# Kernel tuning notes

Measured on AMD Instinct MI355X. Metric: run time of the kernel, lower is better.

Reference implementation:

```python
import jax, jax.numpy as jnp
import numpy as np

D = 1024   # embd_dim
H = 4      # number of SelectiveAttentionModule heads (each full-dim)
B, S = 4, 2048


def _layernorm(x, g, b, eps=1e-5):
    mu = jnp.mean(x, axis=-1, keepdims=True)
    var = jnp.var(x, axis=-1, keepdims=True)
    return (x - mu) * jax.lax.rsqrt(var + eps) * g + b


def setup_inputs() -> dict:
    key = jax.random.key(0)
    ks = jax.random.split(key, 16)
    sd = 1.0 / np.sqrt(D)
    x = jax.random.normal(ks[0], (B, S, D), dtype=jnp.float32)
    # per-head Q/K/V projections, stacked over head dim H ([H, in, out] layout)
    Wq = jax.random.uniform(ks[1], (H, D, D), jnp.float32, -sd, sd)
    bq = jax.random.uniform(ks[2], (H, D), jnp.float32, -sd, sd)
    Wk = jax.random.uniform(ks[3], (H, D, D), jnp.float32, -sd, sd)
    bk = jax.random.uniform(ks[4], (H, D), jnp.float32, -sd, sd)
    Wv = jax.random.uniform(ks[5], (H, D, D), jnp.float32, -sd, sd)
    bv = jax.random.uniform(ks[6], (H, D), jnp.float32, -sd, sd)
    sd1 = 1.0 / np.sqrt(H * D)
    W1 = jax.random.uniform(ks[7], (H * D, D), jnp.float32, -sd1, sd1)  # [in, out]
    b1 = jax.random.uniform(ks[8], (D,), jnp.float32, -sd1, sd1)
    W2 = jax.random.uniform(ks[9], (D, D), jnp.float32, -sd, sd)
    b2 = jax.random.uniform(ks[10], (D,), jnp.float32, -sd, sd)
    g1 = jnp.ones((D,), jnp.float32)
    be1 = jnp.zeros((D,), jnp.float32)
    g2 = jnp.ones((D,), jnp.float32)
    be2 = jnp.zeros((D,), jnp.float32)
    return {"embedding_matrix": x, "Wq": Wq, "bq": bq, "Wk": Wk, "bk": bk,
            "Wv": Wv, "bv": bv, "W1": W1, "b1": b1, "g1": g1, "be1": be1,
            "W2": W2, "b2": b2, "g2": g2, "be2": be2}


def reference(embedding_matrix, Wq, bq, Wk, bk, Wv, bv, W1, b1, g1, be1, W2, b2, g2, be2):
    x = embedding_matrix  # [B, S, D]
    # batched per-head projections: [H, B, S, D]
    q = jnp.einsum('bsd,hde->hbse', x, Wq) + bq[:, None, None, :]
    k = jnp.einsum('bsd,hde->hbse', x, Wk) + bk[:, None, None, :]
    v = jnp.einsum('bsd,hde->hbse', x, Wv) + bv[:, None, None, :]
    scale = 1.0 / jnp.sqrt(jnp.asarray(D, x.dtype))
    scores = jnp.einsum('hbse,hbte->hbst', q, k) * scale  # [H, B, S, S]
    attn = jax.nn.softmax(scores, axis=-1)
    heads = jnp.einsum('hbst,hbte->hbse', attn, v)        # [H, B, S, D]
    # torch.cat([V1..V4], dim=-1) == heads reordered to [B, S, H*D]
    concat = jnp.moveaxis(heads, 0, 2).reshape(x.shape[0], x.shape[1], H * D)
    proj = concat @ W1 + b1                               # [B, S, D]
    y = _layernorm(x + proj, g1, be1)
    return _layernorm(y + (y @ W2 + b2), g2, be2)
```

## Files before the change

### kernel.cpp

```cpp
#include <hip/hip_runtime.h>

using u16 = unsigned short;
using u32 = unsigned int;
typedef __attribute__((ext_vector_type(8))) short s16x8;
typedef __attribute__((ext_vector_type(4))) float f32x4;

typedef uint4   __attribute__((may_alias)) uint4a;
typedef ushort4 __attribute__((may_alias)) ushort4a;
typedef float4  __attribute__((may_alias)) float4a;
typedef u16     __attribute__((may_alias)) u16a;
typedef s16x8   __attribute__((may_alias)) s16x8a;

#define D_ 1024
#define H_ 4
#define B_ 4
#define S_ 2048
#define M_ 8192

#define BM 128
#define BN 128
#define BK 32

__device__ __forceinline__ float bf2f(u16 u) { return __uint_as_float(((u32)u) << 16); }
__device__ __forceinline__ u16 f2bf(float f) {
  u32 b = __float_as_uint(f);
  return (u16)((b + 0x7fffu + ((b >> 16) & 1u)) >> 16);
}

__device__ __forceinline__ void gload_lds16(const u16* g, u16* l) {
  __builtin_amdgcn_global_load_lds(
      (const __attribute__((address_space(1))) void*)g,
      (__attribute__((address_space(3))) void*)l, 16, 0, 0);
}

#define FENCE asm volatile("" ::: "memory")
#define BAR do { FENCE; __builtin_amdgcn_s_barrier(); FENCE; } while (0)
#define VMC8 asm volatile("s_waitcnt vmcnt(8)" ::: "memory")
#define VMC4 asm volatile("s_waitcnt vmcnt(4)" ::: "memory")
#define VMC0 asm volatile("s_waitcnt vmcnt(0)" ::: "memory")
#define LGKM0 do { asm volatile("s_waitcnt lgkmcnt(0)" ::: "memory"); \
                   __builtin_amdgcn_sched_barrier(0); } while (0)

__device__ __forceinline__ void swz_decomp(int& x, int& y, int& z) {
  const int gx = gridDim.x, gy = gridDim.y;
  const int nwg = gx * gy * gridDim.z;
  const int flat = (blockIdx.z * gy + blockIdx.y) * gx + blockIdx.x;
  const int swz = (flat & 7) * (nwg >> 3) + (flat >> 3);
  const int t = swz >> 4, i = swz & 15;
  const int tiles_X = (gx * gridDim.z) >> 2;
  const int X = (t % tiles_X) * 4 + (i & 3);
  y = (t / tiles_X) * 4 + (i >> 2);
  z = X / gx;
  x = X % gx;
}

__global__ __launch_bounds__(256) void cvt_f32_bf16(const float* __restrict__ in,
                                                    u16* __restrict__ out, long n4) {
  long stride = (long)gridDim.x * blockDim.x;
  for (long i = (long)blockIdx.x * blockDim.x + threadIdx.x; i < n4; i += stride) {
    float4 v = ((const float4a*)in)[i];
    ushort4 o;
    o.x = f2bf(v.x); o.y = f2bf(v.y); o.z = f2bf(v.z); o.w = f2bf(v.w);
    ((ushort4a*)out)[i] = o;
  }
}

__global__ __launch_bounds__(256) void tcvt(const float* __restrict__ in,
                                            u16* __restrict__ out, int K, int N,
                                            long s_in, long s_out) {
  __shared__ float t[32][33];
  const int z = blockIdx.z;
  in += (long)z * s_in;
  out += (long)z * s_out;
  const int n0 = blockIdx.x * 32, k0 = blockIdx.y * 32;
  const int tx = threadIdx.x & 31, ty = threadIdx.x >> 5;
#pragma unroll
  for (int i = 0; i < 32; i += 8) t[ty + i][tx] = in[(long)(k0 + ty + i) * N + n0 + tx];
  __syncthreads();
#pragma unroll
  for (int i = 0; i < 32; i += 8)
    out[(long)(n0 + ty + i) * K + k0 + tx] = f2bf(t[tx][ty + i]);
}

__global__ __launch_bounds__(256) void biascat(const float* __restrict__ bq,
                                               const float* __restrict__ bk,
                                               const float* __restrict__ bv,
                                               float* __restrict__ o) {
  int i = blockIdx.x * 256 + threadIdx.x;
  float v = (i < 4096) ? bq[i] : ((i < 8192) ? bk[i - 4096] : bv[i - 8192]);
  o[i] = v;
}

__device__ __forceinline__ s16x8 lds_frag(const u16* buf, int r, int jc) {
  return *(const s16x8a*)&buf[(((r << 3) + (jc ^ (r & 7)))) << 3];
}
__device__ __forceinline__ void readB(const u16* Bbuf, int wc, int lane, s16x8 (&bfr)[4][2]) {
#pragma unroll
  for (int j = 0; j < 4; ++j)
#pragma unroll
    for (int s = 0; s < 2; ++s)
      bfr[j][s] = lds_frag(Bbuf, wc * 64 + j * 16 + (lane & 15), 4 * s + (lane >> 4));
}
__device__ __forceinline__ void readA(const u16* Abuf, int q, int wr, int lane, s16x8 (&afr)[2][2]) {
#pragma unroll
  for (int il = 0; il < 2; ++il)
#pragma unroll
    for (int s = 0; s < 2; ++s)
      afr[il][s] = lds_frag(Abuf, wr * 128 + (q * 2 + il) * 16 + (lane & 15), 4 * s + (lane >> 4));
}
__device__ __forceinline__ void mfma_quad(const s16x8 (&afr)[2][2], const s16x8 (&bfr)[4][2],
                                          f32x4 (&acc)[8][4], int q) {
  __builtin_amdgcn_s_setprio(1);
#pragma unroll
  for (int s = 0; s < 2; ++s)
#pragma unroll
    for (int il = 0; il < 2; ++il)
#pragma unroll
      for (int j = 0; j < 4; ++j)
        acc[q * 2 + il][j] =
            __builtin_amdgcn_mfma_f32_16x16x32_bf16(afr[il][s], bfr[j][s], acc[q * 2 + il][j], 0, 0, 0);
  __builtin_amdgcn_s_setprio(0);
}

template <int MODE>
__device__ __forceinline__ void g256_body(
    const u16* __restrict__ A, const u16* __restrict__ Bm, u16* __restrict__ Cp,
    const float* __restrict__ bias, const float* __restrict__ bias2,
    float* __restrict__ dpart, int ldc, long sA, long sB, long sC) {
  __shared__ u16 Al[2][16384];
  __shared__ u16 Bl[2][16384];
  const int bx = blockIdx.x, by = blockIdx.y, z = blockIdx.z;
  A += (long)z * sA;
  Bm += (long)z * sB;
  const long coff = (long)z * sC;
  const int bm = by * 256, bn = bx * 256;
  const int tid = threadIdx.x;
  const int lane = tid & 63;
  const int w = tid >> 6;
  const int wr = w >> 2, wc = w & 3;
  f32x4 acc[8][4] = {};
  const int nt2 = D_ >> 7;

  auto stage = [&](const u16* src, int b0, u16* lbuf, int h, int kt) {
    const int k0 = kt << 6;
#pragma unroll
    for (int it = 0; it < 2; ++it) {
      int c = w * 128 + it * 64 + lane;
      int row = h * 128 + (c >> 3);
      int j = (c & 7) ^ (row & 7);
      gload_lds16(src + (long)(b0 + row) * D_ + (k0 + j * 8),
                  lbuf + ((h * 1024 + w * 128 + it * 64) << 3));
    }
  };

  stage(A, bm, Al[0], 0, 0);
  stage(A, bm, Al[0], 1, 0);
  stage(Bm, bn, Bl[0], 0, 0);
  stage(Bm, bn, Bl[0], 1, 0);
  stage(Bm, bn, Bl[1], 0, 1);
  stage(Bm, bn, Bl[1], 1, 1);
  VMC4;
  BAR;

  s16x8 bfr[4][2];
  for (int i2 = 0; i2 < nt2; ++i2) {
    const int t = i2 * 2;
    s16x8 afr[2][2];
    readB(Bl[0], wc, lane, bfr);
    readA(Al[0], 0, wr, lane, afr);
    stage(A, bm, Al[1], 0, t + 1);
    BAR;
    mfma_quad(afr, bfr, acc, 0);
    BAR;
    readA(Al[0], 1, wr, lane, afr);
    stage(A, bm, Al[1], 1, t + 1);
    BAR;
    mfma_quad(afr, bfr, acc, 1);
    BAR;
    readA(Al[0], 2, wr, lane, afr);
    stage(Bm, bn, Bl[0], 0, t + 2);
    BAR;
    mfma_quad(afr, bfr, acc, 2);
    BAR;
    readA(Al[0], 3, wr, lane, afr);
    stage(Bm, bn, Bl[0], 1, t + 2);
    BAR;
    mfma_quad(afr, bfr, acc, 3);
    VMC4;
    BAR;
    readB(Bl[1], wc, lane, bfr);
    readA(Al[1], 0, wr, lane, afr);
    stage(A, bm, Al[0], 0, t + 2);
    BAR;
    mfma_quad(afr, bfr, acc, 0);
    BAR;
    readA(Al[1], 1, wr, lane, afr);
    stage(A, bm, Al[0], 1, t + 2);
    BAR;
    mfma_quad(afr, bfr, acc, 1);
    BAR;
    readA(Al[1], 2, wr, lane, afr);
    stage(Bm, bn, Bl[1], 0, t + 3);
    BAR;
    mfma_quad(afr, bfr, acc, 2);
    BAR;
    readA(Al[1], 3, wr, lane, afr);
    stage(Bm, bn, Bl[1], 1, t + 3);
    BAR;
    mfma_quad(afr, bfr, acc, 3);
    VMC4;
    BAR;
  }

  if (MODE == 0) {
    const float* bb = (z == 1) ? bias2 : bias;
#pragma unroll
    for (int i = 0; i < 8; i++) {
      int mbase = bm + wr * 128 + i * 16 + ((lane >> 4) << 2);
#pragma unroll
      for (int j = 0; j < 4; j++) {
        int n = bn + wc * 64 + j * 16 + (lane & 15);
        float bv = bb[n];
#pragma unroll
        for (int r = 0; r < 4; r++)
          ((u16a*)Cp)[coff + (long)(mbase + r) * ldc + n] = f2bf(acc[i][j][r] + bv);
      }
    }
  } else {
#pragma unroll
    for (int i = 0; i < 8; i++) {
      int mbase = bm + wr * 128 + i * 16 + ((lane >> 4) << 2);
#pragma unroll
      for (int r = 0; r < 4; r++) {
        const int mm = mbase + r;
        float rowsum = 0.f;
#pragma unroll
        for (int j = 0; j < 4; j++) {
          int n = bn + wc * 64 + j * 16 + (lane & 15);
          float e = __expf(acc[i][j][r] * 0.03125f);
          ((u16a*)Cp)[coff + (long)mm * ldc + n] = f2bf(e);
          rowsum += e;
        }
        rowsum += __shfl_xor(rowsum, 1, 64);
        rowsum += __shfl_xor(rowsum, 2, 64);
        rowsum += __shfl_xor(rowsum, 4, 64);
        rowsum += __shfl_xor(rowsum, 8, 64);
        if ((lane & 15) == 0)
          dpart[((long)z * 32 + (bx * 4 + wc)) * S_ + mm] = rowsum;
      }
    }
  }
}

__global__ __launch_bounds__(512, 2) void kQK(
    const u16* __restrict__ A, const u16* __restrict__ Bm, u16* __restrict__ Cp,
    const float* __restrict__ bias, const float* __restrict__ bias2,
    float* __restrict__ dpart, int ldc, long sA, long sB, long sC) {
  g256_body<0>(A, Bm, Cp, bias, bias2, dpart, ldc, sA, sB, sC);
}
__global__ __launch_bounds__(512, 2) void kSC(
    const u16* __restrict__ A, const u16* __restrict__ Bm, u16* __restrict__ Cp,
    const float* __restrict__ bias, const float* __restrict__ bias2,
    float* __restrict__ dpart, int ldc, long sA, long sB, long sC) {
  g256_body<1>(A, Bm, Cp, bias, bias2, dpart, ldc, sA, sB, sC);
}

__device__ __forceinline__ int lds_slot(int row, int ks) {
  return row * 4 + (ks ^ ((row >> 1) & 3));
}

template <int OUT_MODE, int HAS_BIAS>
__device__ __forceinline__ void gemm2p_body(
    const u16* __restrict__ A, const u16* __restrict__ Bm, void* __restrict__ Cp,
    const float* __restrict__ bias, float* __restrict__ dpart,
    int K, int lda, int ldb, int ldc,
    long sA, long sB, long sC, long sBias, float scale) {
  __shared__ u16 Al[3][BM * BK];
  __shared__ u16 Bl[3][BN * BK];
  __shared__ float sinv[BM];
  int bx, by, z;
  swz_decomp(bx, by, z);
  A += (long)z * sA;
  Bm += (long)z * sB;
  const long coff = (long)z * sC;
  const int bm = by * BM, bn = bx * BN;
  const int tid = threadIdx.x;
  const int lane = tid & 63;
  const int w = tid >> 6;
  const int wr = w >> 1, wc = w & 1;
  f32x4 acc[4][4] = {};

  auto stage = [&](u16* Ad, u16* Bd, int k0) {
#pragma unroll
    for (int it = 0; it < 2; ++it) {
      const int sbase = w * 128 + it * 64;
      const int slot = sbase + lane;
      const int row = slot >> 2;
      const int j = (slot & 3) ^ ((row >> 1) & 3);
      gload_lds16(A + (long)(bm + row) * lda + (k0 + j * 8), Ad + sbase * 8);
      gload_lds16(Bm + (long)(bn + row) * ldb + (k0 + j * 8), Bd + sbase * 8);
    }
  };

  stage(Al[0], Bl[0], 0);
  stage(Al[1], Bl[1], BK);
  stage(Al[2], Bl[2], 2 * BK);
  VMC8;
  BAR;
  int cur = 0;
  for (int k0 = 0; k0 < K; k0 += BK) {
    const int ks = lane >> 4;
    s16x8 a[4], b[4];
#pragma unroll
    for (int i = 0; i < 4; i++) {
      int row = wr * 64 + i * 16 + (lane & 15);
      a[i] = *(const s16x8a*)&Al[cur][lds_slot(row, ks) * 8];
    }
#pragma unroll
    for (int j = 0; j < 4; j++) {
      int row = wc * 64 + j * 16 + (lane & 15);
      b[j] = *(const s16x8a*)&Bl[cur][lds_slot(row, ks) * 8];
    }
    LGKM0;
    BAR;
    if (k0 + 3 * BK < K) stage(Al[cur], Bl[cur], k0 + 3 * BK);
#pragma unroll
    for (int i = 0; i < 4; i++)
#pragma unroll
      for (int j = 0; j < 4; j++)
        acc[i][j] = __builtin_amdgcn_mfma_f32_16x16x32_bf16(a[i], b[j], acc[i][j], 0, 0, 0);
    if (k0 + 3 * BK < K) { VMC8; }
    else if (k0 + 2 * BK < K) { VMC4; }
    else { VMC0; }
    BAR;
    cur = (cur == 2) ? 0 : cur + 1;
  }

  if (OUT_MODE == 5) {
    if (tid < BM) {
      const int row = bm + tid;
      float s = 0.f;
#pragma unroll
      for (int p = 0; p < 32; ++p) s += dpart[((long)z * 32 + p) * S_ + row];
      sinv[tid] = 1.0f / s;
    }
    __syncthreads();
#pragma unroll
    for (int i = 0; i < 4; i++) {
      int mloc = wr * 64 + i * 16 + ((lane >> 4) << 2);
      float inv[4];
#pragma unroll
      for (int r = 0; r < 4; r++) inv[r] = sinv[mloc + r];
#pragma unroll
      for (int j = 0; j < 4; j++) {
        int n = bn + wc * 64 + j * 16 + (lane & 15);
#pragma unroll
        for (int r = 0; r < 4; r++) {
          ((u16a*)Cp)[coff + (long)(bm + mloc + r) * ldc + n] = f2bf(acc[i][j][r] * inv[r]);
        }
      }
    }
    return;
  }
#pragma unroll
  for (int i = 0; i < 4; i++) {
    int mbase = bm + wr * 64 + i * 16 + ((lane >> 4) << 2);
#pragma unroll
    for (int j = 0; j < 4; j++) {
      int n = bn + wc * 64 + j * 16 + (lane & 15);
      float bv = 0.f;
      if (HAS_BIAS) bv = bias[z * sBias + n];
      if (OUT_MODE == 2) {
        ushort4 o;
        o.x = f2bf(acc[i][j][0] * scale + bv);
        o.y = f2bf(acc[i][j][1] * scale + bv);
        o.z = f2bf(acc[i][j][2] * scale + bv);
        o.w = f2bf(acc[i][j][3] * scale + bv);
        long idx = coff + (long)(mbase >> 11) * ((long)D_ * S_) + (long)n * S_ + (mbase & 2047);
        *(ushort4a*)&((u16a*)Cp)[idx] = o;
      } else {
#pragma unroll
        for (int r = 0; r < 4; r++) {
          float v = acc[i][j][r] * scale + bv;
          long idx = coff + (long)(mbase + r) * ldc + n;
          if (OUT_MODE == 1) {
            ((u16a*)Cp)[idx] = f2bf(v);
          } else if (OUT_MODE == 6) {
            u16a* Cb = (u16a*)Cp;
            Cb[idx] = f2bf(bf2f(Cb[idx]) + v);
          } else {
            ((float*)Cp)[idx] = v;
          }
        }
      }
    }
  }
}

#define GEMM2P_ARGS \
    const u16* __restrict__ A, const u16* __restrict__ Bm, void* __restrict__ Cp, \
    const float* __restrict__ bias, float* __restrict__ dpart, \
    int K, int lda, int ldb, int ldc, long sA, long sB, long sC, long sBias, float scale
#define GEMM2P_FWD A, Bm, Cp, bias, dpart, K, lda, ldb, ldc, sA, sB, sC, sBias, scale

__global__ __launch_bounds__(256, 4) void kV(GEMM2P_ARGS)   { gemm2p_body<2, 1>(GEMM2P_FWD); }
__global__ __launch_bounds__(256, 4) void kPV(GEMM2P_ARGS)  { gemm2p_body<5, 0>(GEMM2P_FWD); }
__global__ __launch_bounds__(256, 4) void kW1a(GEMM2P_ARGS) { gemm2p_body<1, 1>(GEMM2P_FWD); }
__global__ __launch_bounds__(256, 4) void kW1b(GEMM2P_ARGS) { gemm2p_body<6, 0>(GEMM2P_FWD); }
__global__ __launch_bounds__(256, 4) void kW2(GEMM2P_ARGS)  { gemm2p_body<0, 1>(GEMM2P_FWD); }

template <int RBF>
__global__ __launch_bounds__(256) void ln_kernel(
    const float* __restrict__ X, const void* __restrict__ R,
    const float* __restrict__ g, const float* __restrict__ be,
    float* __restrict__ Y, u16* __restrict__ Yb) {
  const long row = blockIdx.x;
  const int t = threadIdx.x, lane = t & 63, w = t >> 6;
  const long base = row * 1024 + t * 4;
  float4 a = *(const float4a*)(X + base);
  float r0, r1, r2, r3;
  if (RBF) {
    ushort4 rb = *(const ushort4a*)((const u16*)R + base);
    r0 = bf2f(rb.x); r1 = bf2f(rb.y); r2 = bf2f(rb.z); r3 = bf2f(rb.w);
  } else {
    float4 b = *(const float4a*)((const float*)R + base);
    r0 = b.x; r1 = b.y; r2 = b.z; r3 = b.w;
  }
  float v0 = a.x + r0, v1 = a.y + r1, v2 = a.z + r2, v3 = a.w + r3;
  float s = v0 + v1 + v2 + v3;
  float q = v0 * v0 + v1 * v1 + v2 * v2 + v3 * v3;
#pragma unroll
  for (int o = 32; o > 0; o >>= 1) { s += __shfl_xor(s, o, 64); q += __shfl_xor(q, o, 64); }
  __shared__ float rs[4], rq[4];
  if (lane == 0) { rs[w] = s; rq[w] = q; }
  __syncthreads();
  s = rs[0] + rs[1] + rs[2] + rs[3];
  q = rq[0] + rq[1] + rq[2] + rq[3];
  const float mu = s * (1.f / 1024.f);
  const float var = q * (1.f / 1024.f) - mu * mu;
  const float rstd = rsqrtf(var + 1e-5f);
  float4 gv = *(const float4a*)(g + t * 4);
  float4 bv = *(const float4a*)(be + t * 4);
  float o0 = (v0 - mu) * rstd * gv.x + bv.x;
  float o1 = (v1 - mu) * rstd * gv.y + bv.y;
  float o2 = (v2 - mu) * rstd * gv.z + bv.z;
  float o3 = (v3 - mu) * rstd * gv.w + bv.w;
  float4 o4; o4.x = o0; o4.y = o1; o4.z = o2; o4.w = o3;
  *(float4a*)(Y + base) = o4;
  if (Yb) {
    ushort4 ob; ob.x = f2bf(o0); ob.y = f2bf(o1); ob.z = f2bf(o2); ob.w = f2bf(o3);
    *(ushort4a*)(Yb + base) = ob;
  }
}

extern "C" void kernel_launch(void* const* d_in, const int* in_sizes, int n_in,
                              void* d_out, int out_size, void* d_ws, size_t ws_size,
                              hipStream_t stream) {
  const float* x   = (const float*)d_in[0];
  const float* Wq  = (const float*)d_in[1];
  const float* bq  = (const float*)d_in[2];
  const float* Wk  = (const float*)d_in[3];
  const float* bk  = (const float*)d_in[4];
  const float* Wv  = (const float*)d_in[5];
  const float* bv  = (const float*)d_in[6];
  const float* W1  = (const float*)d_in[7];
  const float* b1  = (const float*)d_in[8];
  const float* g1  = (const float*)d_in[9];
  const float* be1 = (const float*)d_in[10];
  const float* W2  = (const float*)d_in[11];
  const float* b2  = (const float*)d_in[12];
  const float* g2  = (const float*)d_in[13];
  const float* be2 = (const float*)d_in[14];
  float* out = (float*)d_out;

  const size_t NEED = 170999808ULL;
  if (ws_size < NEED) return;
  char* ws = (char*)d_ws;
  u16* xb  = (u16*)(ws + 0L);
  u16* Wqt = (u16*)(ws + 16777216L);
  u16* Wkt = (u16*)(ws + 25165824L);
  u16* Wvt = (u16*)(ws + 33554432L);
  u16* W1t = (u16*)(ws + 41943040L);
  u16* W2t = (u16*)(ws + 50331648L);
  u16* Qh  = (u16*)(ws + 52428800L);
  u16* Kh  = (u16*)(ws + 69206016L);
  u16* Vt  = (u16*)(ws + 85983232L);
  u16* Sbh = (u16*)(ws + 102760448L);
  u16* Cc2 = (u16*)(ws + 136314880L);
  float* biasQKV = (float*)(ws + 169869312L);
  float* dpart   = (float*)(ws + 169951232L);
  u16* projb = (u16*)out;
  float* y  = (float*)Qh;
  u16*   yb = Vt;
  float* z2 = (float*)Cc2;

  dim3 blk(256);
  {
    long n4 = (long)M_ * D_ / 4;
    hipLaunchKernelGGL(cvt_f32_bf16, dim3(4096), blk, 0, stream, x, xb, n4);
  }
  hipLaunchKernelGGL(tcvt, dim3(32, 32, H_), blk, 0, stream, Wq, Wqt, D_, D_,
                     (long)D_ * D_, (long)D_ * D_);
  hipLaunchKernelGGL(tcvt, dim3(32, 32, H_), blk, 0, stream, Wk, Wkt, D_, D_,
                     (long)D_ * D_, (long)D_ * D_);
  hipLaunchKernelGGL(tcvt, dim3(32, 32, H_), blk, 0, stream, Wv, Wvt, D_, D_,
                     (long)D_ * D_, (long)D_ * D_);
  hipLaunchKernelGGL(tcvt, dim3(32, 128, 1), blk, 0, stream, W1, W1t, H_ * D_, D_, 0L, 0L);
  hipLaunchKernelGGL(tcvt, dim3(32, 32, 1), blk, 0, stream, W2, W2t, D_, D_, 0L, 0L);
  hipLaunchKernelGGL(biascat, dim3(48), blk, 0, stream, bq, bk, bv, biasQKV);

  for (int g = 0; g < 2; ++g) {
    for (int hh = 0; hh < 2; ++hh) {
      const int h = g * 2 + hh;
      const long wo = (long)h * D_ * D_;
      hipLaunchKernelGGL(kQK, dim3(4, 32, 2), dim3(512), 0, stream,
                         xb, Wqt + wo, Qh, biasQKV + (long)h * D_,
                         biasQKV + 4096 + (long)h * D_, (float*)nullptr,
                         D_, 0L, (long)H_ * D_ * D_, (long)M_ * D_);
      hipLaunchKernelGGL(kV, dim3(8, 64, 1), blk, 0, stream,
                         xb, Wvt + wo, (void*)Vt, biasQKV + 8192 + (long)h * D_,
                         (float*)nullptr, D_, D_, D_, D_, 0L, 0L, 0L, 0L, 1.0f);
      hipLaunchKernelGGL(kSC, dim3(8, 8, B_), dim3(512), 0, stream,
                         Qh, Kh, Sbh, (const float*)nullptr, (const float*)nullptr,
                         dpart, S_, (long)S_ * D_, (long)S_ * D_, (long)S_ * S_);
      hipLaunchKernelGGL(kPV, dim3(8, 16, B_), blk, 0, stream,
                         Sbh, Vt, (void*)(Cc2 + (long)hh * D_), (const float*)nullptr, dpart,
                         S_, S_, S_, 2 * D_,
                         (long)S_ * S_, (long)D_ * S_, (long)S_ * 2 * D_, 0L, 1.0f);
    }
    if (g == 0) {
      hipLaunchKernelGGL(kW1a, dim3(8, 64, 1), blk, 0, stream,
                         Cc2, W1t + (long)g * 2 * D_, (void*)projb, b1, (float*)nullptr,
                         2 * D_, 2 * D_, H_ * D_, D_, 0L, 0L, 0L, 0L, 1.0f);
    } else {
      hipLaunchKernelGGL(kW1b, dim3(8, 64, 1), blk, 0, stream,
                         Cc2, W1t + (long)g * 2 * D_, (void*)projb, (const float*)nullptr,
                         (float*)nullptr, 2 * D_, 2 * D_, H_ * D_, D_, 0L, 0L, 0L, 0L, 1.0f);
    }
  }

  hipLaunchKernelGGL((ln_kernel<1>), dim3(M_), blk, 0, stream, x, (const void*)projb,
                     g1, be1, y, yb);

  hipLaunchKernelGGL(kW2, dim3(8, 64, 1), blk, 0, stream,
                     yb, W2t, (void*)z2, b2, (float*)nullptr,
                     D_, D_, D_, D_, 0L, 0L, 0L, 0L, 1.0f);

  hipLaunchKernelGGL((ln_kernel<0>), dim3(M_), blk, 0, stream, y, (const void*)z2,
                     g2, be2, out, (u16*)nullptr);
}
```

Measured before the change: 782.2 us.

## Replace 128x128 GEMM kernel with 256x128 tile, 512-thread pipelined GEMM

The secondary GEMMs (V projection, PV, W1 and W2) move from a 128x128x32 triple-buffered 256-thread kernel to a 256x128 tile with BK=64 and 8 waves. This mirrors the interleaved LDS-read, stage and MFMA schedule of the existing 256x256 kernel. The aim is more data reuse per loaded byte and fewer workgroups. In exchange the grid is smaller, which may underfill the CUs (for example 256 blocks for kV and kW2), and occupancy is lower. The swizzled block ordering is dropped.

```diff
diff --git a/kernel.cpp b/kernel.cpp
--- a/kernel.cpp
+++ b/kernel.cpp
@@ -17,10 +17,6 @@
 #define S_ 2048
 #define M_ 8192
 
-#define BM 128
-#define BN 128
-#define BK 32
-
 __device__ __forceinline__ float bf2f(u16 u) { return __uint_as_float(((u32)u) << 16); }
 __device__ __forceinline__ u16 f2bf(float f) {
   u32 b = __float_as_uint(f);
@@ -35,24 +31,8 @@
 
 #define FENCE asm volatile("" ::: "memory")
 #define BAR do { FENCE; __builtin_amdgcn_s_barrier(); FENCE; } while (0)
-#define VMC8 asm volatile("s_waitcnt vmcnt(8)" ::: "memory")
 #define VMC4 asm volatile("s_waitcnt vmcnt(4)" ::: "memory")
-#define VMC0 asm volatile("s_waitcnt vmcnt(0)" ::: "memory")
-#define LGKM0 do { asm volatile("s_waitcnt lgkmcnt(0)" ::: "memory"); \
-                   __builtin_amdgcn_sched_barrier(0); } while (0)
-
-__device__ __forceinline__ void swz_decomp(int& x, int& y, int& z) {
-  const int gx = gridDim.x, gy = gridDim.y;
-  const int nwg = gx * gy * gridDim.z;
-  const int flat = (blockIdx.z * gy + blockIdx.y) * gx + blockIdx.x;
-  const int swz = (flat & 7) * (nwg >> 3) + (flat >> 3);
-  const int t = swz >> 4, i = swz & 15;
-  const int tiles_X = (gx * gridDim.z) >> 2;
-  const int X = (t % tiles_X) * 4 + (i & 3);
-  y = (t / tiles_X) * 4 + (i >> 2);
-  z = X / gx;
-  x = X % gx;
-}
+#define VMC2 asm volatile("s_waitcnt vmcnt(2)" ::: "memory")
 
 __global__ __launch_bounds__(256) void cvt_f32_bf16(const float* __restrict__ in,
                                                     u16* __restrict__ out, long n4) {
@@ -94,21 +74,22 @@
 __device__ __forceinline__ s16x8 lds_frag(const u16* buf, int r, int jc) {
   return *(const s16x8a*)&buf[(((r << 3) + (jc ^ (r & 7)))) << 3];
 }
-__device__ __forceinline__ void readB(const u16* Bbuf, int wc, int lane, s16x8 (&bfr)[4][2]) {
+__device__ __forceinline__ void readA(const u16* Abuf, int q, int wr, int lane, s16x8 (&afr)[2][2]) {
+#pragma unroll
+  for (int il = 0; il < 2; ++il)
+#pragma unroll
+    for (int s = 0; s < 2; ++s)
+      afr[il][s] = lds_frag(Abuf, wr * 128 + (q * 2 + il) * 16 + (lane & 15), 4 * s + (lane >> 4));
+}
+
+__device__ __forceinline__ void readB256(const u16* Bbuf, int wc, int lane, s16x8 (&bfr)[4][2]) {
 #pragma unroll
   for (int j = 0; j < 4; ++j)
 #pragma unroll
     for (int s = 0; s < 2; ++s)
       bfr[j][s] = lds_frag(Bbuf, wc * 64 + j * 16 + (lane & 15), 4 * s + (lane >> 4));
 }
-__device__ __forceinline__ void readA(const u16* Abuf, int q, int wr, int lane, s16x8 (&afr)[2][2]) {
-#pragma unroll
-  for (int il = 0; il < 2; ++il)
-#pragma unroll
-    for (int s = 0; s < 2; ++s)
-      afr[il][s] = lds_frag(Abuf, wr * 128 + (q * 2 + il) * 16 + (lane & 15), 4 * s + (lane >> 4));
-}
-__device__ __forceinline__ void mfma_quad(const s16x8 (&afr)[2][2], const s16x8 (&bfr)[4][2],
+__device__ __forceinline__ void mfma_q256(const s16x8 (&afr)[2][2], const s16x8 (&bfr)[4][2],
                                           f32x4 (&acc)[8][4], int q) {
   __builtin_amdgcn_s_setprio(1);
 #pragma unroll
@@ -166,48 +147,48 @@
   for (int i2 = 0; i2 < nt2; ++i2) {
     const int t = i2 * 2;
     s16x8 afr[2][2];
-    readB(Bl[0], wc, lane, bfr);
+    readB256(Bl[0], wc, lane, bfr);
     readA(Al[0], 0, wr, lane, afr);
     stage(A, bm, Al[1], 0, t + 1);
     BAR;
-    mfma_quad(afr, bfr, acc, 0);
+    mfma_q256(afr, bfr, acc, 0);
     BAR;
     readA(Al[0], 1, wr, lane, afr);
     stage(A, bm, Al[1], 1, t + 1);
     BAR;
-    mfma_quad(afr, bfr, acc, 1);
+    mfma_q256(afr, bfr, acc, 1);
     BAR;
     readA(Al[0], 2, wr, lane, afr);
     stage(Bm, bn, Bl[0], 0, t + 2);
     BAR;
-    mfma_quad(afr, bfr, acc, 2);
+    mfma_q256(afr, bfr, acc, 2);
     BAR;
     readA(Al[0], 3, wr, lane, afr);
     stage(Bm, bn, Bl[0], 1, t + 2);
     BAR;
-    mfma_quad(afr, bfr, acc, 3);
+    mfma_q256(afr, bfr, acc, 3);
     VMC4;
     BAR;
-    readB(Bl[1], wc, lane, bfr);
+    readB256(Bl[1], wc, lane, bfr);
     readA(Al[1], 0, wr, lane, afr);
     stage(A, bm, Al[0], 0, t + 2);
     BAR;
-    mfma_quad(afr, bfr, acc, 0);
+    mfma_q256(afr, bfr, acc, 0);
     BAR;
     readA(Al[1], 1, wr, lane, afr);
     stage(A, bm, Al[0], 1, t + 2);
     BAR;
-    mfma_quad(afr, bfr, acc, 1);
+    mfma_q256(afr, bfr, acc, 1);
     BAR;
     readA(Al[1], 2, wr, lane, afr);
     stage(Bm, bn, Bl[1], 0, t + 3);
     BAR;
-    mfma_quad(afr, bfr, acc, 2);
+    mfma_q256(afr, bfr, acc, 2);
     BAR;
     readA(Al[1], 3, wr, lane, afr);
     stage(Bm, bn, Bl[1], 1, t + 3);
     BAR;
-    mfma_quad(afr, bfr, acc, 3);
+    mfma_q256(afr, bfr, acc, 3);
     VMC4;
     BAR;
   }
@@ -265,79 +246,127 @@
   g256_body<1>(A, Bm, Cp, bias, bias2, dpart, ldc, sA, sB, sC);
 }
 
-__device__ __forceinline__ int lds_slot(int row, int ks) {
-  return row * 4 + (ks ^ ((row >> 1) & 3));
+__device__ __forceinline__ void readB128(const u16* Bbuf, int wc, int lane, s16x8 (&bfr)[2][2]) {
+#pragma unroll
+  for (int j = 0; j < 2; ++j)
+#pragma unroll
+    for (int s = 0; s < 2; ++s)
+      bfr[j][s] = lds_frag(Bbuf, wc * 32 + j * 16 + (lane & 15), 4 * s + (lane >> 4));
+}
+__device__ __forceinline__ void mfma_q128(const s16x8 (&afr)[2][2], const s16x8 (&bfr)[2][2],
+                                          f32x4 (&acc)[8][2], int q) {
+  __builtin_amdgcn_s_setprio(1);
+#pragma unroll
+  for (int s = 0; s < 2; ++s)
+#pragma unroll
+    for (int il = 0; il < 2; ++il)
+#pragma unroll
+      for (int j = 0; j < 2; ++j)
+        acc[q * 2 + il][j] =
+            __builtin_amdgcn_mfma_f32_16x16x32_bf16(afr[il][s], bfr[j][s], acc[q * 2 + il][j], 0, 0, 0);
+  __builtin_amdgcn_s_setprio(0);
 }
 
 template <int OUT_MODE, int HAS_BIAS>
-__device__ __forceinline__ void gemm2p_body(
+__device__ __forceinline__ void g256n_body(
     const u16* __restrict__ A, const u16* __restrict__ Bm, void* __restrict__ Cp,
     const float* __restrict__ bias, float* __restrict__ dpart,
-    int K, int lda, int ldb, int ldc,
-    long sA, long sB, long sC, long sBias, float scale) {
-  __shared__ u16 Al[3][BM * BK];
-  __shared__ u16 Bl[3][BN * BK];
-  __shared__ float sinv[BM];
-  int bx, by, z;
-  swz_decomp(bx, by, z);
+    int K, int lda, int ldb, int ldc, long sA, long sB, long sC, float scale) {
+  __shared__ u16 Al[2][16384];
+  __shared__ u16 Bl[2][8192];
+  __shared__ float sinv[256];
+  const int bx = blockIdx.x, by = blockIdx.y, z = blockIdx.z;
   A += (long)z * sA;
   Bm += (long)z * sB;
   const long coff = (long)z * sC;
-  const int bm = by * BM, bn = bx * BN;
+  const int bm = by * 256, bn = bx * 128;
   const int tid = threadIdx.x;
   const int lane = tid & 63;
   const int w = tid >> 6;
-  const int wr = w >> 1, wc = w & 1;
-  f32x4 acc[4][4] = {};
-
-  auto stage = [&](u16* Ad, u16* Bd, int k0) {
+  const int wr = w >> 2, wc = w & 3;
+  f32x4 acc[8][2] = {};
+  const int nt2 = K >> 7;
+
+  auto stageA = [&](u16* Abuf, int h, int kt) {
+    const int k0 = kt << 6;
 #pragma unroll
     for (int it = 0; it < 2; ++it) {
-      const int sbase = w * 128 + it * 64;
-      const int slot = sbase + lane;
-      const int row = slot >> 2;
-      const int j = (slot & 3) ^ ((row >> 1) & 3);
-      gload_lds16(A + (long)(bm + row) * lda + (k0 + j * 8), Ad + sbase * 8);
-      gload_lds16(Bm + (long)(bn + row) * ldb + (k0 + j * 8), Bd + sbase * 8);
+      int c = w * 128 + it * 64 + lane;
+      int row = h * 128 + (c >> 3);
+      int j = (c & 7) ^ (row & 7);
+      gload_lds16(A + (long)(bm + row) * lda + (k0 + j * 8),
+                  Abuf + ((h * 1024 + w * 128 + it * 64) << 3));
     }
   };
-
-  stage(Al[0], Bl[0], 0);
-  stage(Al[1], Bl[1], BK);
-  stage(Al[2], Bl[2], 2 * BK);
-  VMC8;
+  auto stageB = [&](u16* Bbuf, int kt) {
+    const int k0 = kt << 6;
+#pragma unroll
+    for (int it = 0; it < 2; ++it) {
+      int c = w * 128 + it * 64 + lane;
+      int row = c >> 3;
+      int j = (c & 7) ^ (row & 7);
+      gload_lds16(Bm + (long)(bn + row) * ldb + (k0 + j * 8),
+                  Bbuf + ((w * 128 + it * 64) << 3));
+    }
+  };
+
+  stageA(Al[0], 0, 0);
+  stageA(Al[0], 1, 0);
+  stageB(Bl[0], 0);
+  stageB(Bl[1], 1);
+  VMC2;
   BAR;
-  int cur = 0;
-  for (int k0 = 0; k0 < K; k0 += BK) {
-    const int ks = lane >> 4;
-    s16x8 a[4], b[4];
-#pragma unroll
-    for (int i = 0; i < 4; i++) {
-      int row = wr * 64 + i * 16 + (lane & 15);
-      a[i] = *(const s16x8a*)&Al[cur][lds_slot(row, ks) * 8];
-    }
-#pragma unroll
-    for (int j = 0; j < 4; j++) {
-      int row = wc * 64 + j * 16 + (lane & 15);
-      b[j] = *(const s16x8a*)&Bl[cur][lds_slot(row, ks) * 8];
-    }
-    LGKM0;
-    BAR;
-    if (k0 + 3 * BK < K) stage(Al[cur], Bl[cur], k0 + 3 * BK);
-#pragma unroll
-    for (int i = 0; i < 4; i++)
-#pragma unroll
-      for (int j = 0; j < 4; j++)
-        acc[i][j] = __builtin_amdgcn_mfma_f32_16x16x32_bf16(a[i], b[j], acc[i][j], 0, 0, 0);
-    if (k0 + 3 * BK < K) { VMC8; }
-    else if (k0 + 2 * BK < K) { VMC4; }
-    else { VMC0; }
-    BAR;
-    cur = (cur == 2) ? 0 : cur + 1;
+
+  s16x8 bfr[2][2];
+  for (int i2 = 0; i2 < nt2; ++i2) {
+    const int t = i2 * 2;
+    s16x8 afr[2][2];
+    readB128(Bl[0], wc, lane, bfr);
+    readA(Al[0], 0, wr, lane, afr);
+    stageA(Al[1], 0, t + 1);
+    BAR;
+    mfma_q128(afr, bfr, acc, 0);
+    BAR;
+    readA(Al[0], 1, wr, lane, afr);
+    stageA(Al[1], 1, t + 1);
+    BAR;
+    mfma_q128(afr, bfr, acc, 1);
+    BAR;
+    readA(Al[0], 2, wr, lane, afr);
+    stageB(Bl[0], t + 2);
+    BAR;
+    mfma_q128(afr, bfr, acc, 2);
+    BAR;
+    readA(Al[0], 3, wr, lane, afr);
+    BAR;
+    mfma_q128(afr, bfr, acc, 3);
+    VMC2;
+    BAR;
+    readB128(Bl[1], wc, lane, bfr);
+    readA(Al[1], 0, wr, lane, afr);
+    stageA(Al[0], 0, t + 2);
+    BAR;
+    mfma_q128(afr, bfr, acc, 0);
+    BAR;
+    readA(Al[1], 1, wr, lane, afr);
+    stageA(Al[0], 1, t + 2);
+    BAR;
+    mfma_q128(afr, bfr, acc, 1);
+    BAR;
+    readA(Al[1], 2, wr, lane, afr);
+    stageB(Bl[1], t + 3);
+    BAR;
+    mfma_q128(afr, bfr, acc, 2);
+    BAR;
+    readA(Al[1], 3, wr, lane, afr);
+    BAR;
+    mfma_q128(afr, bfr, acc, 3);
+    VMC2;
+    BAR;
   }
 
   if (OUT_MODE == 5) {
-    if (tid < BM) {
+    if (tid < 256) {
       const int row = bm + tid;
       float s = 0.f;
 #pragma unroll
@@ -346,14 +375,14 @@
     }
     __syncthreads();
 #pragma unroll
-    for (int i = 0; i < 4; i++) {
-      int mloc = wr * 64 + i * 16 + ((lane >> 4) << 2);
+    for (int i = 0; i < 8; i++) {
+      int mloc = wr * 128 + i * 16 + ((lane >> 4) << 2);
       float inv[4];
 #pragma unroll
       for (int r = 0; r < 4; r++) inv[r] = sinv[mloc + r];
 #pragma unroll
-      for (int j = 0; j < 4; j++) {
-        int n = bn + wc * 64 + j * 16 + (lane & 15);
+      for (int j = 0; j < 2; j++) {
+        int n = bn + wc * 32 + j * 16 + (lane & 15);
 #pragma unroll
         for (int r = 0; r < 4; r++) {
           ((u16a*)Cp)[coff + (long)(bm + mloc + r) * ldc + n] = f2bf(acc[i][j][r] * inv[r]);
@@ -363,13 +392,13 @@
     return;
   }
 #pragma unroll
-  for (int i = 0; i < 4; i++) {
-    int mbase = bm + wr * 64 + i * 16 + ((lane >> 4) << 2);
-#pragma unroll
-    for (int j = 0; j < 4; j++) {
-      int n = bn + wc * 64 + j * 16 + (lane & 15);
+  for (int i = 0; i < 8; i++) {
+    int mbase = bm + wr * 128 + i * 16 + ((lane >> 4) << 2);
+#pragma unroll
+    for (int j = 0; j < 2; j++) {
+      int n = bn + wc * 32 + j * 16 + (lane & 15);
       float bv = 0.f;
-      if (HAS_BIAS) bv = bias[z * sBias + n];
+      if (HAS_BIAS) bv = bias[n];
       if (OUT_MODE == 2) {
         ushort4 o;
         o.x = f2bf(acc[i][j][0] * scale + bv);
@@ -397,17 +426,17 @@
   }
 }
 
-#define GEMM2P_ARGS \
+#define G256N_ARGS \
     const u16* __restrict__ A, const u16* __restrict__ Bm, void* __restrict__ Cp, \
     const float* __restrict__ bias, float* __restrict__ dpart, \
-    int K, int lda, int ldb, int ldc, long sA, long sB, long sC, long sBias, float scale
-#define GEMM2P_FWD A, Bm, Cp, bias, dpart, K, lda, ldb, ldc, sA, sB, sC, sBias, scale
-
-__global__ __launch_bounds__(256, 4) void kV(GEMM2P_ARGS)   { gemm2p_body<2, 1>(GEMM2P_FWD); }
-__global__ __launch_bounds__(256, 4) void kPV(GEMM2P_ARGS)  { gemm2p_body<5, 0>(GEMM2P_FWD); }
-__global__ __launch_bounds__(256, 4) void kW1a(GEMM2P_ARGS) { gemm2p_body<1, 1>(GEMM2P_FWD); }
-__global__ __launch_bounds__(256, 4) void kW1b(GEMM2P_ARGS) { gemm2p_body<6, 0>(GEMM2P_FWD); }
-__global__ __launch_bounds__(256, 4) void kW2(GEMM2P_ARGS)  { gemm2p_body<0, 1>(GEMM2P_FWD); }
+    int K, int lda, int ldb, int ldc, long sA, long sB, long sC, float scale
+#define G256N_FWD A, Bm, Cp, bias, dpart, K, lda, ldb, ldc, sA, sB, sC, scale
+
+__global__ __launch_bounds__(512, 2) void kV(G256N_ARGS)   { g256n_body<2, 1>(G256N_FWD); }
+__global__ __launch_bounds__(512, 2) void kPV(G256N_ARGS)  { g256n_body<5, 0>(G256N_FWD); }
+__global__ __launch_bounds__(512, 2) void kW1a(G256N_ARGS) { g256n_body<1, 1>(G256N_FWD); }
+__global__ __launch_bounds__(512, 2) void kW1b(G256N_ARGS) { g256n_body<6, 0>(G256N_FWD); }
+__global__ __launch_bounds__(512, 2) void kW2(G256N_ARGS)  { g256n_body<0, 1>(G256N_FWD); }
 
 template <int RBF>
 __global__ __launch_bounds__(256) void ln_kernel(
@@ -494,7 +523,7 @@
   u16*   yb = Vt;
   float* z2 = (float*)Cc2;
 
-  dim3 blk(256);
+  dim3 blk(256), blk512(512);
   {
     long n4 = (long)M_ * D_ / 4;
     hipLaunchKernelGGL(cvt_f32_bf16, dim3(4096), blk, 0, stream, x, xb, n4);
@@ -513,38 +542,38 @@
     for (int hh = 0; hh < 2; ++hh) {
       const int h = g * 2 + hh;
       const long wo = (long)h * D_ * D_;
-      hipLaunchKernelGGL(kQK, dim3(4, 32, 2), dim3(512), 0, stream,
+      hipLaunchKernelGGL(kQK, dim3(4, 32, 2), blk512, 0, stream,
                          xb, Wqt + wo, Qh, biasQKV + (long)h * D_,
                          biasQKV + 4096 + (long)h * D_, (float*)nullptr,
                          D_, 0L, (long)H_ * D_ * D_, (long)M_ * D_);
-      hipLaunchKernelGGL(kV, dim3(8, 64, 1), blk, 0, stream,
+      hipLaunchKernelGGL(kV, dim3(8, 32, 1), blk512, 0, stream,
                          xb, Wvt + wo, (void*)Vt, biasQKV + 8192 + (long)h * D_,
-                         (float*)nullptr, D_, D_, D_, D_, 0L, 0L, 0L, 0L, 1.0f);
-      hipLaunchKernelGGL(kSC, dim3(8, 8, B_), dim3(512), 0, stream,
+                         (float*)nullptr, D_, D_, D_, D_, 0L, 0L, 0L, 1.0f);
+      hipLaunchKernelGGL(kSC, dim3(8, 8, B_), blk512, 0, stream,
                          Qh, Kh, Sbh, (const float*)nullptr, (const float*)nullptr,
                          dpart, S_, (long)S_ * D_, (long)S_ * D_, (long)S_ * S_);
-      hipLaunchKernelGGL(kPV, dim3(8, 16, B_), blk, 0, stream,
+      hipLaunchKernelGGL(kPV, dim3(8, 8, B_), blk512, 0, stream,
                          Sbh, Vt, (void*)(Cc2 + (long)hh * D_), (const float*)nullptr, dpart,
                          S_, S_, S_, 2 * D_,
-                         (long)S_ * S_, (long)D_ * S_, (long)S_ * 2 * D_, 0L, 1.0f);
+                         (long)S_ * S_, (long)D_ * S_, (long)S_ * 2 * D_, 1.0f);
     }
     if (g == 0) {
-      hipLaunchKernelGGL(kW1a, dim3(8, 64, 1), blk, 0, stream,
+      hipLaunchKernelGGL(kW1a, dim3(8, 32, 1), blk512, 0, stream,
                          Cc2, W1t + (long)g * 2 * D_, (void*)projb, b1, (float*)nullptr,
-                         2 * D_, 2 * D_, H_ * D_, D_, 0L, 0L, 0L, 0L, 1.0f);
+                         2 * D_, 2 * D_, H_ * D_, D_, 0L, 0L, 0L, 1.0f);
     } else {
-      hipLaunchKernelGGL(kW1b, dim3(8, 64, 1), blk, 0, stream,
+      hipLaunchKernelGGL(kW1b, dim3(8, 32, 1), blk512, 0, stream,
                          Cc2, W1t + (long)g * 2 * D_, (void*)projb, (const float*)nullptr,
-                         (float*)nullptr, 2 * D_, 2 * D_, H_ * D_, D_, 0L, 0L, 0L, 0L, 1.0f);
+                         (float*)nullptr, 2 * D_, 2 * D_, H_ * D_, D_, 0L, 0L, 0L, 1.0f);
     }
   }
 
   hipLaunchKernelGGL((ln_kernel<1>), dim3(M_), blk, 0, stream, x, (const void*)projb,
                      g1, be1, y, yb);
 
-  hipLaunchKernelGGL(kW2, dim3(8, 64, 1), blk, 0, stream,
+  hipLaunchKernelGGL(kW2, dim3(8, 32, 1), blk512, 0, stream,
                      yb, W2t, (void*)z2, b2, (float*)nullptr,
-                     D_, D_, D_, D_, 0L, 0L, 0L, 0L, 1.0f);
+                     D_, D_, D_, D_, 0L, 0L, 0L, 1.0f);
 
   hipLaunchKernelGGL((ln_kernel<0>), dim3(M_), blk, 0, stream, y, (const void*)z2,
                      g2, be2, out, (u16*)nullptr);
```

Measured after the change: 868.3 us. 1.11x slower.
